# Kernel optimization log

Measured on AMD Instinct MI355X. Metric: run time of the kernel, lower is better.

Reference implementation:

```python
import jax, jax.numpy as jnp
import numpy as np

B, D_IN, HD, HN = 16384, 1024, 128, 8
D = HD * HN  # 1024
PROJ = int((4.0 / 3.0) * D)  # 1365
EPS = 1e-5


def setup_inputs() -> dict:
    key = jax.random.key(0)
    ks = jax.random.split(key, 16)
    s = 0.02
    inp = {
        'seq': jax.random.normal(ks[0], (B, D_IN), jnp.float32),
        'c0': jnp.zeros((B, D), jnp.float32),
        'n0': jnp.ones((B, D), jnp.float32),
        'h0': jax.random.normal(ks[1], (B, D), jnp.float32) * 0.1,
        'm0': jnp.zeros((B, D), jnp.float32),
        'ln_w': jnp.ones((D_IN,), jnp.float32),
        'ln_b': jnp.zeros((D_IN,), jnp.float32),
        'Wz': jax.random.normal(ks[2], (D, D_IN), jnp.float32) * s,
        'bz': jnp.zeros((D,), jnp.float32),
        'Wi': jax.random.normal(ks[3], (D, D_IN), jnp.float32) * s,
        'bi': jnp.zeros((D,), jnp.float32),
        'Wo': jax.random.normal(ks[4], (D, D_IN), jnp.float32) * s,
        'bo': jnp.zeros((D,), jnp.float32),
        'Wf': jax.random.normal(ks[5], (D, D_IN), jnp.float32) * s,
        'bf': jnp.zeros((D,), jnp.float32),
        'Rz': jax.random.normal(ks[6], (HN, HD, HD), jnp.float32) * s,
        'Ri': jax.random.normal(ks[7], (HN, HD, HD), jnp.float32) * s,
        'Ro': jax.random.normal(ks[8], (HN, HD, HD), jnp.float32) * s,
        'Rf': jax.random.normal(ks[9], (HN, HD, HD), jnp.float32) * s,
        'gn_w': jnp.ones((D,), jnp.float32),
        'gn_b': jnp.zeros((D,), jnp.float32),
        'up_w': jax.random.normal(ks[10], (2 * PROJ, D), jnp.float32) * s,
        'up_b': jnp.zeros((2 * PROJ,), jnp.float32),
        'down_w': jax.random.normal(ks[11], (D_IN, PROJ), jnp.float32) * s,
        'down_b': jnp.zeros((D_IN,), jnp.float32),
    }
    return inp


def _layernorm(x, w, b):
    mu = jnp.mean(x, axis=-1, keepdims=True)
    var = jnp.mean(jnp.square(x - mu), axis=-1, keepdims=True)
    return (x - mu) * jax.lax.rsqrt(var + EPS) * w + b


def _groupnorm(x, w, b):
    # x: (B, D) -> groups of HD channels per head
    xr = x.reshape(x.shape[0], HN, HD)
    mu = jnp.mean(xr, axis=-1, keepdims=True)
    var = jnp.mean(jnp.square(xr - mu), axis=-1, keepdims=True)
    xn = ((xr - mu) * jax.lax.rsqrt(var + EPS)).reshape(x.shape)
    return xn * w + b


def _block_linear(h, R):
    # block-diagonal recurrence: per-head (HD,HD) matmul
    hr = h.reshape(h.shape[0], HN, HD)
    return jnp.einsum('hed,bhd->bhe', R, hr).reshape(h.shape)


def reference(seq, c0, n0, h0, m0, ln_w, ln_b, Wz, bz, Wi, bi, Wo, bo, Wf, bf,
              Rz, Ri, Ro, Rf, gn_w, gn_b, up_w, up_b, down_w, down_b):
    x_t = _layernorm(seq, ln_w, ln_b)
    x_c = x_t  # use_conv=False default path
    i_t = x_c @ Wi.T + bi + _block_linear(h0, Ri)
    f_t = x_c @ Wf.T + bf + _block_linear(h0, Rf)
    z_t = x_t @ Wz.T + bz + _block_linear(h0, Rz)
    o_t = x_t @ Wo.T + bo + _block_linear(h0, Ro)
    m_t = jnp.maximum(f_t + m0, i_t)
    i_e = jnp.exp(i_t - m_t)
    f_e = jnp.exp(f_t - m_t + m0)
    z_a = jnp.tanh(z_t)
    o_a = jax.nn.sigmoid(o_t)
    c_t = f_e * c0 + i_e * z_a
    n_t = f_e * n0 + i_e
    h_t = o_a * (c_t / n_t)
    out = _groupnorm(h_t, gn_w, gn_b)
    up = out @ up_w.T + up_b
    out1, out2 = jnp.split(up, 2, axis=-1)
    out = out1 + jax.nn.gelu(out2, approximate=False)
    out = out @ down_w.T + down_b
    return (out + seq, c_t, n_t, h_t, m_t)
```

## Files before the change

### kernel.cpp

```cpp
#include <hip/hip_runtime.h>
#include <hip/hip_bf16.h>
#include <cstdint>
#include <type_traits>

typedef __attribute__((ext_vector_type(8))) __bf16 bf16x8;
typedef __attribute__((ext_vector_type(8))) short short8;
typedef __attribute__((ext_vector_type(4))) float f32x4;
using u16 = unsigned short;

template <typename T, typename = void> struct mfma_ok : std::false_type {};
template <typename T>
struct mfma_ok<T, std::void_t<decltype(__builtin_amdgcn_mfma_f32_16x16x32_bf16(
    std::declval<T>(), std::declval<T>(), std::declval<f32x4>(), 0, 0, 0))>>
    : std::true_type {};
using frag_t = std::conditional_t<mfma_ok<bf16x8>::value, bf16x8, short8>;
static_assert(sizeof(frag_t) == 16, "frag must be 4 VGPRs");

template <typename T>
__device__ __forceinline__ f32x4 MFMA(T a, T b, f32x4 c) {
  return __builtin_amdgcn_mfma_f32_16x16x32_bf16(a, b, c, 0, 0, 0);
}

__device__ __forceinline__ void gl_lds16(const u16* g, u16* l) {
  __builtin_amdgcn_global_load_lds(
      (const __attribute__((address_space(1))) unsigned int*)g,
      (__attribute__((address_space(3))) unsigned int*)l, 16, 0, 0);
}

__device__ __forceinline__ u16 f2bf(float v) {
  __hip_bfloat16 h = __float2bfloat16(v);
  return __builtin_bit_cast(u16, h);
}

__device__ __forceinline__ int xcd_swz(int wid, int nwg) {
  return (wid & 7) * (nwg >> 3) + (wid >> 3);
}

__device__ __forceinline__ void gemm256(
    const u16* __restrict__ A, int lda,
    const u16* __restrict__ B, int ldb, int K,
    u16* lds, f32x4 (&acc)[8][4])
{
  const int t = threadIdx.x;
  const int l = t & 63;
  const int w = t >> 6;
  const int wm = w >> 2, wc = w & 3;

  const int sc = (t & 7) ^ ((t >> 3) & 7);
  const u16* gA = A + (t >> 3) * lda + sc * 8;
  const u16* gB = B + (t >> 3) * ldb + sc * 8;

#define STAGE(buf, kt) do {                                   \
    const u16* a_ = gA + (kt) * 64;                           \
    const u16* b_ = gB + (kt) * 64;                           \
    u16* s_ = (buf);                                          \
    gl_lds16(a_,             s_ + w * 512);                   \
    gl_lds16(a_ +  64 * lda, s_ +  4096 + w * 512);           \
    gl_lds16(a_ + 128 * lda, s_ +  8192 + w * 512);           \
    gl_lds16(a_ + 192 * lda, s_ + 12288 + w * 512);           \
    gl_lds16(b_,             s_ + 16384 + w * 512);           \
    gl_lds16(b_ +  64 * ldb, s_ + 20480 + w * 512);           \
    gl_lds16(b_ + 128 * ldb, s_ + 24576 + w * 512);           \
    gl_lds16(b_ + 192 * ldb, s_ + 28672 + w * 512);           \
  } while (0)

  const int lr = l & 15;
  const int lk = l >> 4;
  const int lx = l & 7;
  const int pk0 = ((0 + lk) ^ lx) * 8;
  const int pk1 = ((4 + lk) ^ lx) * 8;
  const int arow0 = (wm * 128 + lr) * 64;
  const int brow0 = 16384 + (wc * 64 + lr) * 64;

  const int nt = K >> 6;

  STAGE(lds, 0);
  asm volatile("s_waitcnt vmcnt(0)" ::: "memory");
  __builtin_amdgcn_s_barrier();

  for (int kt = 0; kt < nt; ++kt) {
    u16* cur = lds + (kt & 1) * 32768;
    u16* nxt = lds + ((kt + 1) & 1) * 32768;
    if (kt + 1 < nt) STAGE(nxt, kt + 1);
    __builtin_amdgcn_sched_barrier(0);
#pragma unroll
    for (int kf = 0; kf < 2; ++kf) {
      const int pk = kf ? pk1 : pk0;
      frag_t a[8], b[4];
#pragma unroll
      for (int fm = 0; fm < 8; ++fm)
        a[fm] = *(const frag_t*)(cur + arow0 + fm * 1024 + pk);
#pragma unroll
      for (int fn = 0; fn < 4; ++fn)
        b[fn] = *(const frag_t*)(cur + brow0 + fn * 1024 + pk);
      __builtin_amdgcn_s_setprio(1);
#pragma unroll
      for (int fn = 0; fn < 4; ++fn)
#pragma unroll
        for (int fm = 0; fm < 8; ++fm)
          acc[fm][fn] = MFMA(a[fm], b[fn], acc[fm][fn]);
      __builtin_amdgcn_s_setprio(0);
    }
    asm volatile("s_waitcnt vmcnt(0)" ::: "memory");
    __builtin_amdgcn_s_barrier();
  }
#undef STAGE
}

__global__ __launch_bounds__(256) void prep_kernel(
    const float* __restrict__ Wi, const float* __restrict__ Wf,
    const float* __restrict__ Wz, const float* __restrict__ Wo,
    const float* __restrict__ Ri, const float* __restrict__ Rf,
    const float* __restrict__ Rz, const float* __restrict__ Ro,
    const float* __restrict__ upw, const float* __restrict__ dnw,
    u16* __restrict__ Wint, u16* __restrict__ Rint,
    u16* __restrict__ upint, u16* __restrict__ dnp)
{
  const int stride = gridDim.x * 256;
  for (int i = blockIdx.x * 256 + threadIdx.x; i < 9043968; i += stride) {
    if (i < 4194304) {
      const int s = i >> 18, v = (i >> 10) & 255, k = i & 1023;
      const int wc = v >> 6, gsel = (v >> 4) & 3, c16 = v & 15;
      const int srcRow = s * 64 + wc * 16 + c16;
      const float* W = (gsel == 0) ? Wi : (gsel == 1) ? Wf : (gsel == 2) ? Wz : Wo;
      Wint[i] = f2bf(W[srcRow * 1024 + k]);
    } else if (i < 4718592) {
      const int j = i - 4194304;
      const int s = j >> 15, v = (j >> 7) & 255, k = j & 127;
      const int wc = v >> 6, gsel = (v >> 4) & 3, c16 = v & 15;
      const int head = s >> 1;
      const int colInHead = (s & 1) * 64 + wc * 16 + c16;
      const float* R = (gsel == 0) ? Ri : (gsel == 1) ? Rf : (gsel == 2) ? Rz : Ro;
      Rint[j] = f2bf(R[head * 16384 + colInHead * 128 + k]);
    } else if (i < 7602176) {
      const int j = i - 4718592;
      const int vcol = j >> 10, k = j & 1023;
      const int tile = vcol >> 8, wc = (vcol >> 6) & 3;
      const int half = (vcol >> 5) & 1, c32 = vcol & 31;
      const int a = tile * 128 + wc * 32 + c32;
      upint[j] = (a < 1365) ? f2bf(upw[(half * 1365 + a) * 1024 + k]) : (u16)0;
    } else {
      const int j = i - 7602176;
      const int row = j / 1408, k = j - row * 1408;
      dnp[j] = (k < 1365) ? f2bf(dnw[row * 1365 + k]) : (u16)0;
    }
  }
}

__global__ __launch_bounds__(256) void ln_kernel(
    const float* __restrict__ seq, const float* __restrict__ h0,
    const float* __restrict__ lnw, const float* __restrict__ lnb,
    u16* __restrict__ xb, u16* __restrict__ h0b)
{
  const int row = blockIdx.x;
  const int t = threadIdx.x;
  const float4 v = ((const float4*)(seq + (size_t)row * 1024))[t];
  float s = v.x + v.y + v.z + v.w;
  float q = v.x * v.x + v.y * v.y + v.z * v.z + v.w * v.w;
#pragma unroll
  for (int o = 32; o >= 1; o >>= 1) { s += __shfl_xor(s, o); q += __shfl_xor(q, o); }
  __shared__ float sm[8];
  const int l = t & 63, w = t >> 6;
  if (l == 0) { sm[w] = s; sm[4 + w] = q; }
  __syncthreads();
  s = sm[0] + sm[1] + sm[2] + sm[3];
  q = sm[4] + sm[5] + sm[6] + sm[7];
  const float mu = s * (1.f / 1024.f);
  const float var = q * (1.f / 1024.f) - mu * mu;
  const float rstd = rsqrtf(var + 1e-5f);
  const float4 wv = ((const float4*)lnw)[t];
  const float4 bv = ((const float4*)lnb)[t];
  ushort4 o4;
  o4.x = f2bf((v.x - mu) * rstd * wv.x + bv.x);
  o4.y = f2bf((v.y - mu) * rstd * wv.y + bv.y);
  o4.z = f2bf((v.z - mu) * rstd * wv.z + bv.z);
  o4.w = f2bf((v.w - mu) * rstd * wv.w + bv.w);
  ((ushort4*)(xb + (size_t)row * 1024))[t] = o4;
  const float4 h = ((const float4*)(h0 + (size_t)row * 1024))[t];
  ushort4 h4;
  h4.x = f2bf(h.x); h4.y = f2bf(h.y); h4.z = f2bf(h.z); h4.w = f2bf(h.w);
  ((ushort4*)(h0b + (size_t)row * 1024))[t] = h4;
}

__global__ __launch_bounds__(512, 2) void gate_kernel(
    const u16* __restrict__ xb, const u16* __restrict__ h0b,
    const u16* __restrict__ Wint, const u16* __restrict__ Rint,
    const float* __restrict__ bi, const float* __restrict__ bfv,
    const float* __restrict__ bz, const float* __restrict__ bo,
    const float* __restrict__ c0, const float* __restrict__ n0i,
    const float* __restrict__ m0,
    float* __restrict__ oc, float* __restrict__ on,
    float* __restrict__ oh, float* __restrict__ om)
{
  __shared__ __align__(16) u16 lds[65536];
  const int wid = xcd_swz(blockIdx.x, 1024);
  const int s = wid & 15;
  const int m0r = (wid >> 4) * 256;
  f32x4 acc[8][4] = {};
  gemm256(xb + (size_t)m0r * 1024, 1024, Wint + s * 262144, 1024, 1024, lds, acc);
  const int head = s >> 1;
  gemm256(h0b + (size_t)m0r * 1024 + head * 128, 1024,
          Rint + s * 32768, 128, 128, lds, acc);

  const int t = threadIdx.x, l = t & 63, w = t >> 6, wm = w >> 2, wc = w & 3;
  const int cc = s * 64 + wc * 16 + (l & 15);
  const float biv = bi[cc], bfvv = bfv[cc], bzv = bz[cc], bov = bo[cc];
#pragma unroll
  for (int fm = 0; fm < 8; ++fm) {
    const int rbase = m0r + wm * 128 + fm * 16 + (l >> 4) * 4;
#pragma unroll
    for (int r = 0; r < 4; ++r) {
      const size_t idx = (size_t)(rbase + r) * 1024 + cc;
      const float it = acc[fm][0][r] + biv;
      const float ft = acc[fm][1][r] + bfvv;
      const float zt = acc[fm][2][r] + bzv;
      const float ot = acc[fm][3][r] + bov;
      const float mp = m0[idx];
      const float mt = fmaxf(ft + mp, it);
      const float ie = __expf(it - mt);
      const float fe = __expf(ft - mt + mp);
      const float ct = fe * c0[idx] + ie * tanhf(zt);
      const float nt = fe * n0i[idx] + ie;
      const float ht = (ct / nt) / (1.f + __expf(-ot));
      oc[idx] = ct; on[idx] = nt; oh[idx] = ht; om[idx] = mt;
    }
  }
}

__global__ __launch_bounds__(256) void gn_kernel(
    const float* __restrict__ h, const float* __restrict__ gw,
    const float* __restrict__ gb, u16* __restrict__ gnb)
{
  const int t = threadIdx.x, l = t & 63, w = t >> 6;
  for (int grp = blockIdx.x * 4 + w; grp < 16384 * 8; grp += gridDim.x * 4) {
    const int b = grp >> 3, hd = grp & 7;
    const float2 v = ((const float2*)(h + b * 1024 + hd * 128))[l];
    float s = v.x + v.y, q = v.x * v.x + v.y * v.y;
#pragma unroll
    for (int o = 32; o >= 1; o >>= 1) { s += __shfl_xor(s, o); q += __shfl_xor(q, o); }
    const float mu = s * (1.f / 128.f);
    const float var = q * (1.f / 128.f) - mu * mu;
    const float rstd = rsqrtf(var + 1e-5f);
    const float2 wv = ((const float2*)(gw + hd * 128))[l];
    const float2 bv = ((const float2*)(gb + hd * 128))[l];
    ushort2 o2;
    o2.x = f2bf((v.x - mu) * rstd * wv.x + bv.x);
    o2.y = f2bf((v.y - mu) * rstd * wv.y + bv.y);
    ((ushort2*)(gnb + b * 1024 + hd * 128))[l] = o2;
  }
}

__global__ __launch_bounds__(512, 2) void up_kernel(
    const u16* __restrict__ gnb, const u16* __restrict__ upint,
    const float* __restrict__ upb, u16* __restrict__ g)
{
  __shared__ __align__(16) u16 lds[65536];
  const int wid = xcd_swz(blockIdx.x, 704);
  const int vt = wid % 11, mt = wid / 11;
  const int m0r = mt * 256;
  f32x4 acc[8][4] = {};
  gemm256(gnb + (size_t)m0r * 1024, 1024, upint + vt * 262144, 1024, 1024,
          lds, acc);
  const int t = threadIdx.x, l = t & 63, w = t >> 6, wm = w >> 2, wc = w & 3;
#pragma unroll
  for (int fm = 0; fm < 8; ++fm) {
    const int rbase = m0r + wm * 128 + fm * 16 + (l >> 4) * 4;
#pragma unroll
    for (int fn = 0; fn < 2; ++fn) {
      const int a = vt * 128 + wc * 32 + fn * 16 + (l & 15);
      const float b1 = (a < 1365) ? upb[a] : 0.f;
      const float b2 = (a < 1365) ? upb[1365 + a] : 0.f;
#pragma unroll
      for (int r = 0; r < 4; ++r) {
        const float u1 = acc[fm][fn][r] + b1;
        const float u2 = acc[fm][fn + 2][r] + b2;
        const float ge = 0.5f * u2 * (1.f + erff(u2 * 0.70710678118654752f));
        g[(size_t)(rbase + r) * 1408 + a] = f2bf(u1 + ge);
      }
    }
  }
}

__global__ __launch_bounds__(512, 2) void down_kernel(
    const u16* __restrict__ g, const u16* __restrict__ dnp,
    const float* __restrict__ dnb, const float* __restrict__ seq,
    float* __restrict__ out)
{
  __shared__ __align__(16) u16 lds[65536];
  const int wid = xcd_swz(blockIdx.x, 256);
  const int nc = (wid & 3) * 256;
  const int m0r = (wid >> 2) * 256;
  f32x4 acc[8][4] = {};
  gemm256(g + (size_t)m0r * 1408, 1408, dnp + nc * 1408, 1408, 1408, lds, acc);
  const int t = threadIdx.x, l = t & 63, w = t >> 6, wm = w >> 2, wc = w & 3;
#pragma unroll
  for (int fm = 0; fm < 8; ++fm) {
    const int rbase = m0r + wm * 128 + fm * 16 + (l >> 4) * 4;
#pragma unroll
    for (int fn = 0; fn < 4; ++fn) {
      const int cc = nc + wc * 64 + fn * 16 + (l & 15);
      const float bb = dnb[cc];
#pragma unroll
      for (int r = 0; r < 4; ++r) {
        const size_t idx = (size_t)(rbase + r) * 1024 + cc;
        out[idx] = acc[fm][fn][r] + bb + seq[idx];
      }
    }
  }
}

extern "C" void kernel_launch(void* const* d_in, const int* in_sizes, int n_in,
                              void* d_out, int out_size, void* d_ws, size_t ws_size,
                              hipStream_t stream) {
  const float* seq = (const float*)d_in[0];
  const float* c0  = (const float*)d_in[1];
  const float* n0i = (const float*)d_in[2];
  const float* h0  = (const float*)d_in[3];
  const float* m0  = (const float*)d_in[4];
  const float* lnw = (const float*)d_in[5];
  const float* lnb = (const float*)d_in[6];
  const float* Wz  = (const float*)d_in[7];
  const float* bz  = (const float*)d_in[8];
  const float* Wi  = (const float*)d_in[9];
  const float* bi  = (const float*)d_in[10];
  const float* Wo  = (const float*)d_in[11];
  const float* bo  = (const float*)d_in[12];
  const float* Wf  = (const float*)d_in[13];
  const float* bf_ = (const float*)d_in[14];
  const float* Rz  = (const float*)d_in[15];
  const float* Ri  = (const float*)d_in[16];
  const float* Ro  = (const float*)d_in[17];
  const float* Rf  = (const float*)d_in[18];
  const float* gw  = (const float*)d_in[19];
  const float* gb  = (const float*)d_in[20];
  const float* upw = (const float*)d_in[21];
  const float* upb = (const float*)d_in[22];
  const float* dnw = (const float*)d_in[23];
  const float* dnb = (const float*)d_in[24];

  char* ws = (char*)d_ws;
  u16* xb   = (u16*)(ws);
  u16* h0b  = (u16*)(ws + 33554432);
  u16* Wint = (u16*)(ws + 67108864);
  u16* Rint = (u16*)(ws + 75497472);
  u16* upc  = (u16*)(ws + 76546048);
  u16* dnp  = (u16*)(ws + 82313216);
  u16* g    = (u16*)(ws + 85196800);

  float* out = (float*)d_out;
  float* oc = out + 16777216;
  float* on = out + 2 * 16777216;
  float* oh = out + 3 * 16777216;
  float* om = out + 4 * 16777216;

  prep_kernel<<<dim3(2048), dim3(256), 0, stream>>>(
      Wi, Wf, Wz, Wo, Ri, Rf, Rz, Ro, upw, dnw, Wint, Rint, upc, dnp);
  ln_kernel<<<dim3(16384), dim3(256), 0, stream>>>(seq, h0, lnw, lnb, xb, h0b);
  gate_kernel<<<dim3(1024), dim3(512), 0, stream>>>(
      xb, h0b, Wint, Rint, bi, bf_, bz, bo, c0, n0i, m0, oc, on, oh, om);
  gn_kernel<<<dim3(2048), dim3(256), 0, stream>>>(oh, gw, gb, xb);
  up_kernel<<<dim3(704), dim3(512), 0, stream>>>(xb, upc, upb, g);
  down_kernel<<<dim3(256), dim3(512), 0, stream>>>(g, dnp, dnb, seq, out);
}
```

Baseline: 505.9 us.

## Split GEMM k-step into four quadrant phases interleaving LDS reads and staging

```diff
diff --git a/kernel.cpp b/kernel.cpp
--- a/kernel.cpp
+++ b/kernel.cpp
@@ -50,20 +50,6 @@
   const u16* gA = A + (t >> 3) * lda + sc * 8;
   const u16* gB = B + (t >> 3) * ldb + sc * 8;
 
-#define STAGE(buf, kt) do {                                   \
-    const u16* a_ = gA + (kt) * 64;                           \
-    const u16* b_ = gB + (kt) * 64;                           \
-    u16* s_ = (buf);                                          \
-    gl_lds16(a_,             s_ + w * 512);                   \
-    gl_lds16(a_ +  64 * lda, s_ +  4096 + w * 512);           \
-    gl_lds16(a_ + 128 * lda, s_ +  8192 + w * 512);           \
-    gl_lds16(a_ + 192 * lda, s_ + 12288 + w * 512);           \
-    gl_lds16(b_,             s_ + 16384 + w * 512);           \
-    gl_lds16(b_ +  64 * ldb, s_ + 20480 + w * 512);           \
-    gl_lds16(b_ + 128 * ldb, s_ + 24576 + w * 512);           \
-    gl_lds16(b_ + 192 * ldb, s_ + 28672 + w * 512);           \
-  } while (0)
-
   const int lr = l & 15;
   const int lk = l >> 4;
   const int lx = l & 7;
@@ -74,37 +60,110 @@
 
   const int nt = K >> 6;
 
-  STAGE(lds, 0);
+#define STAGE_A(buf, kt) do {                                  \
+    const u16* a_ = gA + (kt) * 64;                            \
+    u16* s_ = (buf);                                           \
+    gl_lds16(a_,             s_ + w * 512);                    \
+    gl_lds16(a_ +  64 * lda, s_ +  4096 + w * 512);            \
+    gl_lds16(a_ + 128 * lda, s_ +  8192 + w * 512);            \
+    gl_lds16(a_ + 192 * lda, s_ + 12288 + w * 512);            \
+  } while (0)
+#define STAGE_B(buf, kt) do {                                  \
+    const u16* b_ = gB + (kt) * 64;                            \
+    u16* s_ = (buf);                                           \
+    gl_lds16(b_,             s_ + 16384 + w * 512);            \
+    gl_lds16(b_ +  64 * ldb, s_ + 20480 + w * 512);            \
+    gl_lds16(b_ + 128 * ldb, s_ + 24576 + w * 512);            \
+    gl_lds16(b_ + 192 * ldb, s_ + 28672 + w * 512);            \
+  } while (0)
+
+  STAGE_A(lds, 0);
+  STAGE_B(lds, 0);
   asm volatile("s_waitcnt vmcnt(0)" ::: "memory");
   __builtin_amdgcn_s_barrier();
 
   for (int kt = 0; kt < nt; ++kt) {
     u16* cur = lds + (kt & 1) * 32768;
     u16* nxt = lds + ((kt + 1) & 1) * 32768;
-    if (kt + 1 < nt) STAGE(nxt, kt + 1);
-    __builtin_amdgcn_sched_barrier(0);
-#pragma unroll
-    for (int kf = 0; kf < 2; ++kf) {
-      const int pk = kf ? pk1 : pk0;
-      frag_t a[8], b[4];
-#pragma unroll
-      for (int fm = 0; fm < 8; ++fm)
-        a[fm] = *(const frag_t*)(cur + arow0 + fm * 1024 + pk);
-#pragma unroll
-      for (int fn = 0; fn < 4; ++fn)
-        b[fn] = *(const frag_t*)(cur + brow0 + fn * 1024 + pk);
-      __builtin_amdgcn_s_setprio(1);
-#pragma unroll
-      for (int fn = 0; fn < 4; ++fn)
-#pragma unroll
-        for (int fm = 0; fm < 8; ++fm)
-          acc[fm][fn] = MFMA(a[fm], b[fn], acc[fm][fn]);
-      __builtin_amdgcn_s_setprio(0);
-    }
-    asm volatile("s_waitcnt vmcnt(0)" ::: "memory");
-    __builtin_amdgcn_s_barrier();
-  }
-#undef STAGE
+    const bool more = (kt + 1 < nt);
+
+    frag_t aL[8], aH[8], bL[4], bH[4];
+
+#pragma unroll
+    for (int fm = 0; fm < 4; ++fm) {
+      aL[2 * fm]     = *(const frag_t*)(cur + arow0 + fm * 1024 + pk0);
+      aL[2 * fm + 1] = *(const frag_t*)(cur + arow0 + fm * 1024 + pk1);
+    }
+#pragma unroll
+    for (int fn = 0; fn < 2; ++fn) {
+      bL[2 * fn]     = *(const frag_t*)(cur + brow0 + fn * 1024 + pk0);
+      bL[2 * fn + 1] = *(const frag_t*)(cur + brow0 + fn * 1024 + pk1);
+    }
+    if (more) STAGE_A(nxt, kt + 1);
+    __builtin_amdgcn_s_barrier();
+    __builtin_amdgcn_s_setprio(1);
+#pragma unroll
+    for (int fn = 0; fn < 2; ++fn)
+#pragma unroll
+      for (int fm = 0; fm < 4; ++fm)
+#pragma unroll
+        for (int kf = 0; kf < 2; ++kf)
+          acc[fm][fn] = MFMA(aL[2 * fm + kf], bL[2 * fn + kf], acc[fm][fn]);
+    __builtin_amdgcn_s_setprio(0);
+    __builtin_amdgcn_s_barrier();
+
+#pragma unroll
+    for (int fn = 0; fn < 2; ++fn) {
+      bH[2 * fn]     = *(const frag_t*)(cur + brow0 + (fn + 2) * 1024 + pk0);
+      bH[2 * fn + 1] = *(const frag_t*)(cur + brow0 + (fn + 2) * 1024 + pk1);
+    }
+    if (more) STAGE_B(nxt, kt + 1);
+    __builtin_amdgcn_s_barrier();
+    __builtin_amdgcn_s_setprio(1);
+#pragma unroll
+    for (int fn = 0; fn < 2; ++fn)
+#pragma unroll
+      for (int fm = 0; fm < 4; ++fm)
+#pragma unroll
+        for (int kf = 0; kf < 2; ++kf)
+          acc[fm][fn + 2] =
+              MFMA(aL[2 * fm + kf], bH[2 * fn + kf], acc[fm][fn + 2]);
+    __builtin_amdgcn_s_setprio(0);
+    __builtin_amdgcn_s_barrier();
+
+#pragma unroll
+    for (int fm = 0; fm < 4; ++fm) {
+      aH[2 * fm]     = *(const frag_t*)(cur + arow0 + (fm + 4) * 1024 + pk0);
+      aH[2 * fm + 1] = *(const frag_t*)(cur + arow0 + (fm + 4) * 1024 + pk1);
+    }
+    __builtin_amdgcn_s_barrier();
+    __builtin_amdgcn_s_setprio(1);
+#pragma unroll
+    for (int fn = 0; fn < 2; ++fn)
+#pragma unroll
+      for (int fm = 0; fm < 4; ++fm)
+#pragma unroll
+        for (int kf = 0; kf < 2; ++kf)
+          acc[fm + 4][fn + 2] =
+              MFMA(aH[2 * fm + kf], bH[2 * fn + kf], acc[fm + 4][fn + 2]);
+    __builtin_amdgcn_s_setprio(0);
+    __builtin_amdgcn_s_barrier();
+
+    __builtin_amdgcn_s_setprio(1);
+#pragma unroll
+    for (int fn = 0; fn < 2; ++fn)
+#pragma unroll
+      for (int fm = 0; fm < 4; ++fm)
+#pragma unroll
+        for (int kf = 0; kf < 2; ++kf)
+          acc[fm + 4][fn] =
+              MFMA(aH[2 * fm + kf], bL[2 * fn + kf], acc[fm + 4][fn]);
+    __builtin_amdgcn_s_setprio(0);
+    if (more) asm volatile("s_waitcnt vmcnt(0)" ::: "memory");
+    __builtin_amdgcn_s_barrier();
+  }
+#undef STAGE_A
+#undef STAGE_B
 }
 
 __global__ __launch_bounds__(256) void prep_kernel(
```

Measured after the change: 512.0 us. Within noise of the previous version (+1.2%).

## Halve GEMM K-tile to 32 and shrink LDS to 64KB per block

Applied to the files above, without the earlier changes.

```diff
diff --git a/kernel.cpp b/kernel.cpp
--- a/kernel.cpp
+++ b/kernel.cpp
@@ -46,65 +46,59 @@
   const int w = t >> 6;
   const int wm = w >> 2, wc = w & 3;
 
-  const int sc = (t & 7) ^ ((t >> 3) & 7);
-  const u16* gA = A + (t >> 3) * lda + sc * 8;
-  const u16* gB = B + (t >> 3) * ldb + sc * 8;
-
-#define STAGE(buf, kt) do {                                   \
-    const u16* a_ = gA + (kt) * 64;                           \
-    const u16* b_ = gB + (kt) * 64;                           \
-    u16* s_ = (buf);                                          \
-    gl_lds16(a_,             s_ + w * 512);                   \
-    gl_lds16(a_ +  64 * lda, s_ +  4096 + w * 512);           \
-    gl_lds16(a_ + 128 * lda, s_ +  8192 + w * 512);           \
-    gl_lds16(a_ + 192 * lda, s_ + 12288 + w * 512);           \
-    gl_lds16(b_,             s_ + 16384 + w * 512);           \
-    gl_lds16(b_ +  64 * ldb, s_ + 20480 + w * 512);           \
-    gl_lds16(b_ + 128 * ldb, s_ + 24576 + w * 512);           \
-    gl_lds16(b_ + 192 * ldb, s_ + 28672 + w * 512);           \
+  const int sr = t >> 2;
+  const int cs = (t & 3) ^ ((sr & 3) ^ ((sr >> 2) & 3));
+  const u16* gA = A + sr * lda + cs * 8;
+  const u16* gB = B + sr * ldb + cs * 8;
+
+  const int lr = l & 15;
+  const int kceff = (l >> 4) ^ ((l & 3) ^ ((l >> 2) & 3));
+  const int abase = wm * 4096 + lr * 32 + kceff * 8;
+  const int bbase = 8192 + wc * 2048 + lr * 32 + kceff * 8;
+
+  const int nt = K >> 5;
+
+#define STG(buf, kt) do {                                      \
+    u16* s_ = (buf);                                           \
+    const u16* a_ = gA + (kt) * 32;                            \
+    const u16* b_ = gB + (kt) * 32;                            \
+    gl_lds16(a_,             s_ + w * 512);                    \
+    gl_lds16(a_ + 128 * lda, s_ +  4096 + w * 512);            \
+    gl_lds16(b_,             s_ +  8192 + w * 512);            \
+    gl_lds16(b_ + 128 * ldb, s_ + 12288 + w * 512);            \
   } while (0)
 
-  const int lr = l & 15;
-  const int lk = l >> 4;
-  const int lx = l & 7;
-  const int pk0 = ((0 + lk) ^ lx) * 8;
-  const int pk1 = ((4 + lk) ^ lx) * 8;
-  const int arow0 = (wm * 128 + lr) * 64;
-  const int brow0 = 16384 + (wc * 64 + lr) * 64;
-
-  const int nt = K >> 6;
-
-  STAGE(lds, 0);
+  STG(lds, 0);
   asm volatile("s_waitcnt vmcnt(0)" ::: "memory");
   __builtin_amdgcn_s_barrier();
 
   for (int kt = 0; kt < nt; ++kt) {
-    u16* cur = lds + (kt & 1) * 32768;
-    u16* nxt = lds + ((kt + 1) & 1) * 32768;
-    if (kt + 1 < nt) STAGE(nxt, kt + 1);
-    __builtin_amdgcn_sched_barrier(0);
-#pragma unroll
-    for (int kf = 0; kf < 2; ++kf) {
-      const int pk = kf ? pk1 : pk0;
-      frag_t a[8], b[4];
+    u16* cur = lds + (kt & 1) * 16384;
+    u16* nxt = lds + ((kt + 1) & 1) * 16384;
+    const bool more = (kt + 1 < nt);
+    if (more) STG(nxt, kt + 1);
+
+    frag_t a[8], b[4];
+#pragma unroll
+    for (int fm = 0; fm < 8; ++fm)
+      a[fm] = *(const frag_t*)(cur + abase + fm * 512);
+#pragma unroll
+    for (int fn = 0; fn < 4; ++fn)
+      b[fn] = *(const frag_t*)(cur + bbase + fn * 512);
+
+    __builtin_amdgcn_s_setprio(1);
+#pragma unroll
+    for (int fn = 0; fn < 4; ++fn)
 #pragma unroll
       for (int fm = 0; fm < 8; ++fm)
-        a[fm] = *(const frag_t*)(cur + arow0 + fm * 1024 + pk);
-#pragma unroll
-      for (int fn = 0; fn < 4; ++fn)
-        b[fn] = *(const frag_t*)(cur + brow0 + fn * 1024 + pk);
-      __builtin_amdgcn_s_setprio(1);
-#pragma unroll
-      for (int fn = 0; fn < 4; ++fn)
-#pragma unroll
-        for (int fm = 0; fm < 8; ++fm)
-          acc[fm][fn] = MFMA(a[fm], b[fn], acc[fm][fn]);
-      __builtin_amdgcn_s_setprio(0);
-    }
-    asm volatile("s_waitcnt vmcnt(0)" ::: "memory");
+        acc[fm][fn] = MFMA(a[fm], b[fn], acc[fm][fn]);
+    __builtin_amdgcn_s_setprio(0);
+
+    if (more) asm volatile("s_waitcnt vmcnt(0)" ::: "memory");
+    else      asm volatile("" ::: "memory");
     __builtin_amdgcn_s_barrier();
   }
-#undef STAGE
+#undef STG
 }
 
 __global__ __launch_bounds__(256) void prep_kernel(
@@ -192,7 +186,7 @@
     float* __restrict__ oc, float* __restrict__ on,
     float* __restrict__ oh, float* __restrict__ om)
 {
-  __shared__ __align__(16) u16 lds[65536];
+  __shared__ __align__(16) u16 lds[32768];
   const int wid = xcd_swz(blockIdx.x, 1024);
   const int s = wid & 15;
   const int m0r = (wid >> 4) * 256;
@@ -254,7 +248,7 @@
     const u16* __restrict__ gnb, const u16* __restrict__ upint,
     const float* __restrict__ upb, u16* __restrict__ g)
 {
-  __shared__ __align__(16) u16 lds[65536];
+  __shared__ __align__(16) u16 lds[32768];
   const int wid = xcd_swz(blockIdx.x, 704);
   const int vt = wid % 11, mt = wid / 11;
   const int m0r = mt * 256;
@@ -286,7 +280,7 @@
     const float* __restrict__ dnb, const float* __restrict__ seq,
     float* __restrict__ out)
 {
-  __shared__ __align__(16) u16 lds[65536];
+  __shared__ __align__(16) u16 lds[32768];
   const int wid = xcd_swz(blockIdx.x, 256);
   const int nc = (wid & 3) * 256;
   const int m0r = (wid >> 2) * 256;
```

New measurement: 546.3 us. 1.08x slower.

## Fuse weight prep with layernorm, concatenate W/R along K, retile gate GEMM

Applied to the files above, without the earlier changes.

```diff
diff --git a/kernel.cpp b/kernel.cpp
--- a/kernel.cpp
+++ b/kernel.cpp
@@ -49,6 +49,16 @@
   const int sc = (t & 7) ^ ((t >> 3) & 7);
   const u16* gA = A + (t >> 3) * lda + sc * 8;
   const u16* gB = B + (t >> 3) * ldb + sc * 8;
+
+  const int lr = l & 15;
+  const int lk = l >> 4;
+  const int lx = l & 7;
+  const int pk0 = ((0 + lk) ^ lx) * 8;
+  const int pk1 = ((4 + lk) ^ lx) * 8;
+  const int arow0 = (wm * 128 + lr) * 64;
+  const int brow0 = 16384 + (wc * 64 + lr) * 64;
+
+  const int nt = K >> 6;
 
 #define STAGE(buf, kt) do {                                   \
     const u16* a_ = gA + (kt) * 64;                           \
@@ -64,16 +74,6 @@
     gl_lds16(b_ + 192 * ldb, s_ + 28672 + w * 512);           \
   } while (0)
 
-  const int lr = l & 15;
-  const int lk = l >> 4;
-  const int lx = l & 7;
-  const int pk0 = ((0 + lk) ^ lx) * 8;
-  const int pk1 = ((4 + lk) ^ lx) * 8;
-  const int arow0 = (wm * 128 + lr) * 64;
-  const int brow0 = 16384 + (wc * 64 + lr) * 64;
-
-  const int nt = K >> 6;
-
   STAGE(lds, 0);
   asm volatile("s_waitcnt vmcnt(0)" ::: "memory");
   __builtin_amdgcn_s_barrier();
@@ -107,31 +107,68 @@
 #undef STAGE
 }
 
-__global__ __launch_bounds__(256) void prep_kernel(
+__global__ __launch_bounds__(256) void prep_ln_kernel(
+    const float* __restrict__ seq, const float* __restrict__ h0,
+    const float* __restrict__ lnw, const float* __restrict__ lnb,
     const float* __restrict__ Wi, const float* __restrict__ Wf,
     const float* __restrict__ Wz, const float* __restrict__ Wo,
     const float* __restrict__ Ri, const float* __restrict__ Rf,
     const float* __restrict__ Rz, const float* __restrict__ Ro,
     const float* __restrict__ upw, const float* __restrict__ dnw,
-    u16* __restrict__ Wint, u16* __restrict__ Rint,
-    u16* __restrict__ upint, u16* __restrict__ dnp)
-{
-  const int stride = gridDim.x * 256;
-  for (int i = blockIdx.x * 256 + threadIdx.x; i < 9043968; i += stride) {
-    if (i < 4194304) {
-      const int s = i >> 18, v = (i >> 10) & 255, k = i & 1023;
-      const int wc = v >> 6, gsel = (v >> 4) & 3, c16 = v & 15;
-      const int srcRow = s * 64 + wc * 16 + c16;
-      const float* W = (gsel == 0) ? Wi : (gsel == 1) ? Wf : (gsel == 2) ? Wz : Wo;
-      Wint[i] = f2bf(W[srcRow * 1024 + k]);
-    } else if (i < 4718592) {
-      const int j = i - 4194304;
-      const int s = j >> 15, v = (j >> 7) & 255, k = j & 127;
-      const int wc = v >> 6, gsel = (v >> 4) & 3, c16 = v & 15;
-      const int head = s >> 1;
-      const int colInHead = (s & 1) * 64 + wc * 16 + c16;
-      const float* R = (gsel == 0) ? Ri : (gsel == 1) ? Rf : (gsel == 2) ? Rz : Ro;
-      Rint[j] = f2bf(R[head * 16384 + colInHead * 128 + k]);
+    u16* __restrict__ xb, u16* __restrict__ h0b,
+    u16* __restrict__ Wcat2, u16* __restrict__ upint, u16* __restrict__ dnp)
+{
+  const int t = threadIdx.x;
+  if (blockIdx.x < 16384) {
+    const int row = blockIdx.x;
+    const float4 v = ((const float4*)(seq + (size_t)row * 1024))[t];
+    float s = v.x + v.y + v.z + v.w;
+    float q = v.x * v.x + v.y * v.y + v.z * v.z + v.w * v.w;
+#pragma unroll
+    for (int o = 32; o >= 1; o >>= 1) { s += __shfl_xor(s, o); q += __shfl_xor(q, o); }
+    __shared__ float sm[8];
+    const int l = t & 63, w = t >> 6;
+    if (l == 0) { sm[w] = s; sm[4 + w] = q; }
+    __syncthreads();
+    s = sm[0] + sm[1] + sm[2] + sm[3];
+    q = sm[4] + sm[5] + sm[6] + sm[7];
+    const float mu = s * (1.f / 1024.f);
+    const float var = q * (1.f / 1024.f) - mu * mu;
+    const float rstd = rsqrtf(var + 1e-5f);
+    const float4 wv = ((const float4*)lnw)[t];
+    const float4 bv = ((const float4*)lnb)[t];
+    ushort4 o4;
+    o4.x = f2bf((v.x - mu) * rstd * wv.x + bv.x);
+    o4.y = f2bf((v.y - mu) * rstd * wv.y + bv.y);
+    o4.z = f2bf((v.z - mu) * rstd * wv.z + bv.z);
+    o4.w = f2bf((v.w - mu) * rstd * wv.w + bv.w);
+    ((ushort4*)(xb + (size_t)row * 1024))[t] = o4;
+    const float4 h = ((const float4*)(h0 + (size_t)row * 1024))[t];
+    ushort4 h4;
+    h4.x = f2bf(h.x); h4.y = f2bf(h.y); h4.z = f2bf(h.z); h4.w = f2bf(h.w);
+    ((ushort4*)(h0b + (size_t)row * 1024))[t] = h4;
+    return;
+  }
+  const int stride = 2048 * 256;
+  for (int i = (blockIdx.x - 16384) * 256 + t; i < 9043968; i += stride) {
+    if (i < 4718592) {
+      const int s = i / 294912;
+      const int rem = i - s * 294912;
+      const int vcol = rem / 1152;
+      const int k = rem - vcol * 1152;
+      const int wc = vcol >> 6, gsel = (vcol >> 4) & 3, c16 = vcol & 15;
+      float v;
+      if (k < 1024) {
+        const int col = s * 64 + wc * 16 + c16;
+        const float* W = (gsel == 0) ? Wi : (gsel == 1) ? Wf : (gsel == 2) ? Wz : Wo;
+        v = W[col * 1024 + k];
+      } else {
+        const int head = s >> 1;
+        const int colInHead = (s & 1) * 64 + wc * 16 + c16;
+        const float* R = (gsel == 0) ? Ri : (gsel == 1) ? Rf : (gsel == 2) ? Rz : Ro;
+        v = R[head * 16384 + colInHead * 128 + (k - 1024)];
+      }
+      Wcat2[i] = f2bf(v);
     } else if (i < 7602176) {
       const int j = i - 4718592;
       const int vcol = j >> 10, k = j & 1023;
@@ -147,44 +184,9 @@
   }
 }
 
-__global__ __launch_bounds__(256) void ln_kernel(
-    const float* __restrict__ seq, const float* __restrict__ h0,
-    const float* __restrict__ lnw, const float* __restrict__ lnb,
-    u16* __restrict__ xb, u16* __restrict__ h0b)
-{
-  const int row = blockIdx.x;
-  const int t = threadIdx.x;
-  const float4 v = ((const float4*)(seq + (size_t)row * 1024))[t];
-  float s = v.x + v.y + v.z + v.w;
-  float q = v.x * v.x + v.y * v.y + v.z * v.z + v.w * v.w;
-#pragma unroll
-  for (int o = 32; o >= 1; o >>= 1) { s += __shfl_xor(s, o); q += __shfl_xor(q, o); }
-  __shared__ float sm[8];
-  const int l = t & 63, w = t >> 6;
-  if (l == 0) { sm[w] = s; sm[4 + w] = q; }
-  __syncthreads();
-  s = sm[0] + sm[1] + sm[2] + sm[3];
-  q = sm[4] + sm[5] + sm[6] + sm[7];
-  const float mu = s * (1.f / 1024.f);
-  const float var = q * (1.f / 1024.f) - mu * mu;
-  const float rstd = rsqrtf(var + 1e-5f);
-  const float4 wv = ((const float4*)lnw)[t];
-  const float4 bv = ((const float4*)lnb)[t];
-  ushort4 o4;
-  o4.x = f2bf((v.x - mu) * rstd * wv.x + bv.x);
-  o4.y = f2bf((v.y - mu) * rstd * wv.y + bv.y);
-  o4.z = f2bf((v.z - mu) * rstd * wv.z + bv.z);
-  o4.w = f2bf((v.w - mu) * rstd * wv.w + bv.w);
-  ((ushort4*)(xb + (size_t)row * 1024))[t] = o4;
-  const float4 h = ((const float4*)(h0 + (size_t)row * 1024))[t];
-  ushort4 h4;
-  h4.x = f2bf(h.x); h4.y = f2bf(h.y); h4.z = f2bf(h.z); h4.w = f2bf(h.w);
-  ((ushort4*)(h0b + (size_t)row * 1024))[t] = h4;
-}
-
-__global__ __launch_bounds__(512, 2) void gate_kernel(
+__global__ __launch_bounds__(256, 2) void gate_kernel(
     const u16* __restrict__ xb, const u16* __restrict__ h0b,
-    const u16* __restrict__ Wint, const u16* __restrict__ Rint,
+    const u16* __restrict__ Wcat2,
     const float* __restrict__ bi, const float* __restrict__ bfv,
     const float* __restrict__ bz, const float* __restrict__ bo,
     const float* __restrict__ c0, const float* __restrict__ n0i,
@@ -192,22 +194,73 @@
     float* __restrict__ oc, float* __restrict__ on,
     float* __restrict__ oh, float* __restrict__ om)
 {
-  __shared__ __align__(16) u16 lds[65536];
-  const int wid = xcd_swz(blockIdx.x, 1024);
+  __shared__ __align__(16) u16 lds[24576];
+  const int t = threadIdx.x;
+  const int l = t & 63;
+  const int w = t >> 6;
+
+  const int wid = xcd_swz(blockIdx.x, 2048);
   const int s = wid & 15;
-  const int m0r = (wid >> 4) * 256;
+  const int mt = wid >> 4;
+  const int head = s >> 1;
+
+  const u16* Agl = xb + (size_t)mt * 131072;
+  const u16* Hgl = h0b + (size_t)mt * 131072 + head * 128;
+  const u16* Bgl = Wcat2 + s * 294912;
+
+  const int gsw = ((t & 3) ^ ((t >> 3) & 3)) * 8;
+  const int sr = t >> 2;
+
+  const int lr = l & 15, lk = l >> 4;
+  const int ck = (lk ^ ((lr >> 1) & 3)) * 8;
+
   f32x4 acc[8][4] = {};
-  gemm256(xb + (size_t)m0r * 1024, 1024, Wint + s * 262144, 1024, 1024, lds, acc);
-  const int head = s >> 1;
-  gemm256(h0b + (size_t)m0r * 1024 + head * 128, 1024,
-          Rint + s * 32768, 128, 128, lds, acc);
-
-  const int t = threadIdx.x, l = t & 63, w = t >> 6, wm = w >> 2, wc = w & 3;
-  const int cc = s * 64 + wc * 16 + (l & 15);
+
+#define GSTG(buf, kt) do {                                                 \
+    const u16* Ab = ((kt) < 32) ? (Agl + (kt) * 32) : (Hgl + ((kt) - 32) * 32); \
+    const u16* Bb = Bgl + (kt) * 32;                                       \
+    u16* s_ = (buf);                                                       \
+    gl_lds16(Ab + sr * 1024 + gsw,          s_ + w * 512);                 \
+    gl_lds16(Ab + (64 + sr) * 1024 + gsw,   s_ + 2048 + w * 512);          \
+    gl_lds16(Bb + sr * 1152 + gsw,          s_ + 4096 + w * 512);          \
+    gl_lds16(Bb + (64 + sr) * 1152 + gsw,   s_ + 6144 + w * 512);          \
+    gl_lds16(Bb + (128 + sr) * 1152 + gsw,  s_ + 8192 + w * 512);          \
+    gl_lds16(Bb + (192 + sr) * 1152 + gsw,  s_ + 10240 + w * 512);         \
+  } while (0)
+
+  GSTG(lds, 0);
+  asm volatile("s_waitcnt vmcnt(0)" ::: "memory");
+  __builtin_amdgcn_s_barrier();
+
+  for (int kt = 0; kt < 36; ++kt) {
+    u16* cur = lds + (kt & 1) * 12288;
+    u16* nxt = lds + ((kt + 1) & 1) * 12288;
+    const bool more = (kt + 1 < 36);
+    if (more) GSTG(nxt, kt + 1);
+
+    frag_t a[8], b[4];
+#pragma unroll
+    for (int fm = 0; fm < 8; ++fm)
+      a[fm] = *(const frag_t*)(cur + (fm * 16 + lr) * 32 + ck);
+#pragma unroll
+    for (int fn = 0; fn < 4; ++fn)
+      b[fn] = *(const frag_t*)(cur + 4096 + (w * 64 + fn * 16 + lr) * 32 + ck);
+#pragma unroll
+    for (int fn = 0; fn < 4; ++fn)
+#pragma unroll
+      for (int fm = 0; fm < 8; ++fm)
+        acc[fm][fn] = MFMA(a[fm], b[fn], acc[fm][fn]);
+
+    if (more) asm volatile("s_waitcnt vmcnt(0)" ::: "memory");
+    __builtin_amdgcn_s_barrier();
+  }
+#undef GSTG
+
+  const int cc = s * 64 + w * 16 + lr;
   const float biv = bi[cc], bfvv = bfv[cc], bzv = bz[cc], bov = bo[cc];
 #pragma unroll
   for (int fm = 0; fm < 8; ++fm) {
-    const int rbase = m0r + wm * 128 + fm * 16 + (l >> 4) * 4;
+    const int rbase = mt * 128 + fm * 16 + lk * 4;
 #pragma unroll
     for (int r = 0; r < 4; ++r) {
       const size_t idx = (size_t)(rbase + r) * 1024 + cc;
@@ -216,13 +269,13 @@
       const float zt = acc[fm][2][r] + bzv;
       const float ot = acc[fm][3][r] + bov;
       const float mp = m0[idx];
-      const float mt = fmaxf(ft + mp, it);
-      const float ie = __expf(it - mt);
-      const float fe = __expf(ft - mt + mp);
+      const float mt_ = fmaxf(ft + mp, it);
+      const float ie = __expf(it - mt_);
+      const float fe = __expf(ft - mt_ + mp);
       const float ct = fe * c0[idx] + ie * tanhf(zt);
       const float nt = fe * n0i[idx] + ie;
       const float ht = (ct / nt) / (1.f + __expf(-ot));
-      oc[idx] = ct; on[idx] = nt; oh[idx] = ht; om[idx] = mt;
+      oc[idx] = ct; on[idx] = nt; oh[idx] = ht; om[idx] = mt_;
     }
   }
 }
@@ -339,13 +392,12 @@
   const float* dnb = (const float*)d_in[24];
 
   char* ws = (char*)d_ws;
-  u16* xb   = (u16*)(ws);
-  u16* h0b  = (u16*)(ws + 33554432);
-  u16* Wint = (u16*)(ws + 67108864);
-  u16* Rint = (u16*)(ws + 75497472);
-  u16* upc  = (u16*)(ws + 76546048);
-  u16* dnp  = (u16*)(ws + 82313216);
-  u16* g    = (u16*)(ws + 85196800);
+  u16* xb    = (u16*)(ws);
+  u16* h0b   = (u16*)(ws + 33554432);
+  u16* Wcat2 = (u16*)(ws + 67108864);
+  u16* upc   = (u16*)(ws + 76546048);
+  u16* dnp   = (u16*)(ws + 82313216);
+  u16* g     = (u16*)(ws + 85196800);
 
   float* out = (float*)d_out;
   float* oc = out + 16777216;
@@ -353,11 +405,11 @@
   float* oh = out + 3 * 16777216;
   float* om = out + 4 * 16777216;
 
-  prep_kernel<<<dim3(2048), dim3(256), 0, stream>>>(
-      Wi, Wf, Wz, Wo, Ri, Rf, Rz, Ro, upw, dnw, Wint, Rint, upc, dnp);
-  ln_kernel<<<dim3(16384), dim3(256), 0, stream>>>(seq, h0, lnw, lnb, xb, h0b);
-  gate_kernel<<<dim3(1024), dim3(512), 0, stream>>>(
-      xb, h0b, Wint, Rint, bi, bf_, bz, bo, c0, n0i, m0, oc, on, oh, om);
+  prep_ln_kernel<<<dim3(18432), dim3(256), 0, stream>>>(
+      seq, h0, lnw, lnb, Wi, Wf, Wz, Wo, Ri, Rf, Rz, Ro, upw, dnw,
+      xb, h0b, Wcat2, upc, dnp);
+  gate_kernel<<<dim3(2048), dim3(256), 0, stream>>>(
+      xb, h0b, Wcat2, bi, bf_, bz, bo, c0, n0i, m0, oc, on, oh, om);
   gn_kernel<<<dim3(2048), dim3(256), 0, stream>>>(oh, gw, gb, xb);
   up_kernel<<<dim3(704), dim3(512), 0, stream>>>(xb, upc, upb, g);
   down_kernel<<<dim3(256), dim3(512), 0, stream>>>(g, dnp, dnb, seq, out);
```

Result: slower. 525.6 us (+3.9%).
